# Kernel optimization log

Hardware: AMD Instinct MI355X
Metric: run time of the kernel (lower is better)

The kernel has to match this reference:

```python
import jax, jax.numpy as jnp
import numpy as np

SQRT_D = 32  # ceil(sqrt(d_out)) with d_out = 1024
D_OUT = 1024


def setup_inputs() -> dict:
    key = jax.random.key(0)
    k1, k2, k3 = jax.random.split(key, 3)
    x = jax.random.normal(k1, (8, 4096, 1024), dtype=jnp.float32)
    scale = 1.0 / np.sqrt(SQRT_D)
    L = jax.random.normal(k2, (SQRT_D, SQRT_D, SQRT_D), dtype=jnp.float32) * scale
    R = jax.random.normal(k3, (SQRT_D, SQRT_D, SQRT_D), dtype=jnp.float32) * scale
    return {"x": x, "L": L, "R": R}


def reference(x, L, R):
    # MonarchOutProjection with proj_type == 'Monarch' (d_in*n_heads == d_out,
    # hd == sqrt_d**2 so no padding). Monarch: permute -> blockdiag(L) ->
    # permute -> blockdiag(R) -> permute, then slice to d_out.
    b, n, hd = x.shape
    s = SQRT_D
    # rearrange '... (m n) -> ... (n m)': view (m, n) then transpose.
    h = x.reshape(b, n, s, s)          # (..., m, n_inner)
    h = jnp.swapaxes(h, -1, -2)        # (..., block, inner)
    # blockdiag_matmul with L: einsum 'bnm,...bm->...bn'
    h = jnp.einsum('bnm,...bm->...bn', L, h)
    # rearrange '... (m n) -> ... (n m)' on the flattened result == transpose
    h = jnp.swapaxes(h, -1, -2)
    # blockdiag_matmul with R
    h = jnp.einsum('bnm,...bm->...bn', R, h)
    # final rearrange '... (m n) -> ... (n m)'
    h = jnp.swapaxes(h, -1, -2)
    out = h.reshape(b, n, hd)
    return out[..., :D_OUT]
```

## Files before the change

kernel.cpp:

```cpp
#include <hip/hip_runtime.h>
#include <hip/hip_bf16.h>


typedef __attribute__((ext_vector_type(8))) short short8;
typedef __attribute__((ext_vector_type(4))) float floatx4;

__device__ __forceinline__ unsigned int f2bf(float f) {
    unsigned int u = __float_as_uint(f);
    return (u + 0x7fffu + ((u >> 16) & 1u)) >> 16;
}
__device__ __forceinline__ unsigned int pack2bf(float a, float b) {
    __hip_bfloat162 h = __float22bfloat162_rn(float2{a, b});
    return *(unsigned int*)&h;
}
__device__ __forceinline__ float bf2f(unsigned int u16) {
    return __uint_as_float(u16 << 16);
}

__global__ void prep_weights(const float* __restrict__ L, const float* __restrict__ R,
                             unsigned short* __restrict__ Lb, unsigned short* __restrict__ Rb) {
    const int t = blockIdx.x * 256 + threadIdx.x;
    const float* src        = (t < 4096) ? L : R;
    unsigned short* dst     = (t < 4096) ? Lb : Rb;
    const int i    = t & 4095;
    const int lane = i & 63;
    const int pq   = i >> 6;
    const int p    = pq >> 1;
    const int qt   = pq & 1;
    const int q    = qt * 16 + (lane & 15);
    const int m0   = (lane >> 4) * 8;
    const float* s = src + (p * 32 + q) * 32 + m0;
    uint4 o;
    o.x = pack2bf(s[0], s[1]);
    o.y = pack2bf(s[2], s[3]);
    o.z = pack2bf(s[4], s[5]);
    o.w = pack2bf(s[6], s[7]);
    *(uint4*)(dst + (size_t)i * 8) = o;
}

__global__ __launch_bounds__(256, 4)
void monarch_kernel(const float* __restrict__ x,
                    const unsigned short* __restrict__ Lb,
                    const unsigned short* __restrict__ Rb,
                    float* __restrict__ out) {
    __shared__ __align__(16) unsigned short buf[16][1024];

    const int tid  = threadIdx.x;
    const int w    = tid >> 6;
    const int lane = tid & 63;
    const int tl   = lane & 15;
    const int quad = lane >> 4;
    const long tok0 = (long)blockIdx.x * 16;

    {
        const int c = tid * 4;
        #pragma unroll
        for (int t = 0; t < 16; ++t) {
            const float4 v = *(const float4*)(x + (tok0 + t) * 1024 + c);
            *(unsigned int*)&buf[t][(c    ) ^ (2 * t)] = pack2bf(v.x, v.y);
            *(unsigned int*)&buf[t][(c + 2) ^ (2 * t)] = pack2bf(v.z, v.w);
        }
    }
    __syncthreads();

    {
        const int xsw = 2 * tl;
        #pragma unroll
        for (int pp = 0; pp < 8; ++pp) {
            const int p  = w * 8 + pp;
            const int pX = p ^ xsw;
            short8 b1;
            #pragma unroll
            for (int j = 0; j < 8; ++j)
                b1[j] = (short)buf[tl][quad * 256 + j * 32 + pX];
            #pragma unroll
            for (int qt = 0; qt < 2; ++qt) {
                const short8 a1 = *(const short8*)(Lb + (size_t)((p * 2 + qt) * 64 + lane) * 8);
                floatx4 acc = {0.f, 0.f, 0.f, 0.f};
                acc = __builtin_amdgcn_mfma_f32_16x16x32_bf16(a1, b1, acc, 0, 0, 0);
                #pragma unroll
                for (int r = 0; r < 4; ++r) {
                    const int qo = qt * 16 + quad * 4 + r;
                    buf[tl][qo * 32 + pX] = (unsigned short)f2bf(acc[r]);
                }
            }
        }
    }
    __syncthreads();

    floatx4 acc2[8][2];
    {
        const int xsw = 2 * tl;
        #pragma unroll
        for (int qq = 0; qq < 8; ++qq) {
            const int q = w * 8 + qq;
            short8 b2;
            #pragma unroll
            for (int j = 0; j < 8; ++j)
                b2[j] = (short)buf[tl][q * 32 + ((quad * 8 + j) ^ xsw)];
            #pragma unroll
            for (int rt = 0; rt < 2; ++rt) {
                const short8 a2 = *(const short8*)(Rb + (size_t)((q * 2 + rt) * 64 + lane) * 8);
                floatx4 z = {0.f, 0.f, 0.f, 0.f};
                acc2[qq][rt] = __builtin_amdgcn_mfma_f32_16x16x32_bf16(a2, b2, z, 0, 0, 0);
            }
        }
    }
    __syncthreads();

    {
        const int xsw = 2 * tl;
        #pragma unroll
        for (int qq = 0; qq < 8; ++qq) {
            const int q  = w * 8 + qq;
            const int qX = q ^ xsw;
            #pragma unroll
            for (int rt = 0; rt < 2; ++rt) {
                #pragma unroll
                for (int r4 = 0; r4 < 4; ++r4) {
                    const int ro = rt * 16 + quad * 4 + r4;
                    buf[tl][ro * 32 + qX] = (unsigned short)f2bf(acc2[qq][rt][r4]);
                }
            }
        }
    }
    __syncthreads();

    {
        const int c = tid * 4;
        #pragma unroll
        for (int t = 0; t < 16; ++t) {
            const unsigned int u0 = *(const unsigned int*)&buf[t][(c    ) ^ (2 * t)];
            const unsigned int u1 = *(const unsigned int*)&buf[t][(c + 2) ^ (2 * t)];
            float4 o;
            o.x = bf2f(u0 & 0xffffu); o.y = bf2f(u0 >> 16);
            o.z = bf2f(u1 & 0xffffu); o.w = bf2f(u1 >> 16);
            *(float4*)(out + (tok0 + t) * 1024 + c) = o;
        }
    }
}

extern "C" void kernel_launch(void* const* d_in, const int* in_sizes, int n_in,
                              void* d_out, int out_size, void* d_ws, size_t ws_size,
                              hipStream_t stream) {
    const float* x = (const float*)d_in[0];
    const float* L = (const float*)d_in[1];
    const float* R = (const float*)d_in[2];
    float* out = (float*)d_out;

    unsigned short* Lb = (unsigned short*)d_ws;
    unsigned short* Rb = Lb + 32768;

    prep_weights<<<32, 256, 0, stream>>>(L, R, Lb, Rb);

    const int n_tokens = 8 * 4096;
    const int grid = n_tokens / 16;
    monarch_kernel<<<grid, 256, 0, stream>>>(x, Lb, Rb, out);
}
```

Before: 241.6 us.

## Persist blocks over four token tiles with register prefetch and dual LDS buffers

```diff
diff --git a/kernel.cpp b/kernel.cpp
--- a/kernel.cpp
+++ b/kernel.cpp
@@ -5,16 +5,15 @@
 typedef __attribute__((ext_vector_type(8))) short short8;
 typedef __attribute__((ext_vector_type(4))) float floatx4;
 
-__device__ __forceinline__ unsigned int f2bf(float f) {
-    unsigned int u = __float_as_uint(f);
-    return (u + 0x7fffu + ((u >> 16) & 1u)) >> 16;
-}
 __device__ __forceinline__ unsigned int pack2bf(float a, float b) {
     __hip_bfloat162 h = __float22bfloat162_rn(float2{a, b});
     return *(unsigned int*)&h;
 }
-__device__ __forceinline__ float bf2f(unsigned int u16) {
-    return __uint_as_float(u16 << 16);
+
+__device__ __forceinline__ void block_sync() {
+    asm volatile("s_waitcnt lgkmcnt(0)" ::: "memory");
+    __builtin_amdgcn_s_barrier();
+    asm volatile("" ::: "memory");
 }
 
 __global__ void prep_weights(const float* __restrict__ L, const float* __restrict__ R,
@@ -38,105 +37,129 @@
     *(uint4*)(dst + (size_t)i * 8) = o;
 }
 
-__global__ __launch_bounds__(256, 4)
+#define TILES 4
+
+__global__ __launch_bounds__(256, 2)
 void monarch_kernel(const float* __restrict__ x,
                     const unsigned short* __restrict__ Lb,
                     const unsigned short* __restrict__ Rb,
                     float* __restrict__ out) {
-    __shared__ __align__(16) unsigned short buf[16][1024];
+    __shared__ __align__(16) unsigned short bufX[16][1024];
+    __shared__ __align__(16) unsigned short bufY[16][1024];
 
     const int tid  = threadIdx.x;
     const int w    = tid >> 6;
     const int lane = tid & 63;
     const int tl   = lane & 15;
     const int quad = lane >> 4;
-    const long tok0 = (long)blockIdx.x * 16;
+    const int c    = tid * 4;
 
+    short8 ra[8][2];
+    #pragma unroll
+    for (int qq = 0; qq < 8; ++qq) {
+        const int q = w * 8 + qq;
+        ra[qq][0] = *(const short8*)(Rb + (size_t)((q * 2 + 0) * 64 + lane) * 8);
+        ra[qq][1] = *(const short8*)(Rb + (size_t)((q * 2 + 1) * 64 + lane) * 8);
+    }
+
+    const long tile0 = (long)blockIdx.x * TILES;
+
+    float4 xr[16];
     {
-        const int c = tid * 4;
+        const long tok0 = tile0 * 16;
+        #pragma unroll
+        for (int t = 0; t < 16; ++t)
+            xr[t] = *(const float4*)(x + (tok0 + t) * 1024 + c);
+    }
+
+    for (int it = 0; it < TILES; ++it) {
+        const long tok0 = (tile0 + it) * 16;
+
+        short8 la[8][2];
+        #pragma unroll
+        for (int pp = 0; pp < 8; ++pp) {
+            const int p = w * 8 + pp;
+            la[pp][0] = *(const short8*)(Lb + (size_t)((p * 2 + 0) * 64 + lane) * 8);
+            la[pp][1] = *(const short8*)(Lb + (size_t)((p * 2 + 1) * 64 + lane) * 8);
+        }
+
         #pragma unroll
         for (int t = 0; t < 16; ++t) {
-            const float4 v = *(const float4*)(x + (tok0 + t) * 1024 + c);
-            *(unsigned int*)&buf[t][(c    ) ^ (2 * t)] = pack2bf(v.x, v.y);
-            *(unsigned int*)&buf[t][(c + 2) ^ (2 * t)] = pack2bf(v.z, v.w);
+            const unsigned long long v =
+                ((unsigned long long)pack2bf(xr[t].z, xr[t].w) << 32) | pack2bf(xr[t].x, xr[t].y);
+            *(unsigned long long*)&bufX[t][c ^ (t << 2)] = v;
         }
-    }
-    __syncthreads();
+        block_sync();
 
-    {
-        const int xsw = 2 * tl;
+        short8 b1[8];
         #pragma unroll
         for (int pp = 0; pp < 8; ++pp) {
-            const int p  = w * 8 + pp;
-            const int pX = p ^ xsw;
-            short8 b1;
+            const int p = w * 8 + pp;
             #pragma unroll
             for (int j = 0; j < 8; ++j)
-                b1[j] = (short)buf[tl][quad * 256 + j * 32 + pX];
+                b1[pp][j] = (short)bufX[tl][(quad * 256 + j * 32 + p) ^ (tl << 2)];
+        }
+        #pragma unroll
+        for (int pp = 0; pp < 8; ++pp) {
+            const int p = w * 8 + pp;
             #pragma unroll
             for (int qt = 0; qt < 2; ++qt) {
-                const short8 a1 = *(const short8*)(Lb + (size_t)((p * 2 + qt) * 64 + lane) * 8);
                 floatx4 acc = {0.f, 0.f, 0.f, 0.f};
-                acc = __builtin_amdgcn_mfma_f32_16x16x32_bf16(a1, b1, acc, 0, 0, 0);
-                #pragma unroll
-                for (int r = 0; r < 4; ++r) {
-                    const int qo = qt * 16 + quad * 4 + r;
-                    buf[tl][qo * 32 + pX] = (unsigned short)f2bf(acc[r]);
-                }
+                acc = __builtin_amdgcn_mfma_f32_16x16x32_bf16(la[pp][qt], b1[pp], acc, 0, 0, 0);
+                const unsigned long long v =
+                    ((unsigned long long)pack2bf(acc[2], acc[3]) << 32) | pack2bf(acc[0], acc[1]);
+                const int el = p * 32 + qt * 16 + quad * 4;
+                *(unsigned long long*)&bufY[tl][el ^ (tl << 2)] = v;
             }
         }
-    }
-    __syncthreads();
+        block_sync();
 
-    floatx4 acc2[8][2];
-    {
-        const int xsw = 2 * tl;
+        short8 b2[8];
         #pragma unroll
         for (int qq = 0; qq < 8; ++qq) {
             const int q = w * 8 + qq;
-            short8 b2;
             #pragma unroll
             for (int j = 0; j < 8; ++j)
-                b2[j] = (short)buf[tl][q * 32 + ((quad * 8 + j) ^ xsw)];
+                b2[qq][j] = (short)bufY[tl][((quad * 8 + j) * 32 + q) ^ (tl << 2)];
+        }
+        if (it + 1 < TILES) {
+            const long ntok0 = (tile0 + it + 1) * 16;
+            #pragma unroll
+            for (int t = 0; t < 16; ++t)
+                xr[t] = *(const float4*)(x + (ntok0 + t) * 1024 + c);
+        }
+        #pragma unroll
+        for (int qq = 0; qq < 8; ++qq) {
+            const int q = w * 8 + qq;
             #pragma unroll
             for (int rt = 0; rt < 2; ++rt) {
-                const short8 a2 = *(const short8*)(Rb + (size_t)((q * 2 + rt) * 64 + lane) * 8);
                 floatx4 z = {0.f, 0.f, 0.f, 0.f};
-                acc2[qq][rt] = __builtin_amdgcn_mfma_f32_16x16x32_bf16(a2, b2, z, 0, 0, 0);
+                const floatx4 acc =
+                    __builtin_amdgcn_mfma_f32_16x16x32_bf16(ra[qq][rt], b2[qq], z, 0, 0, 0);
+                const unsigned int lo = pack2bf(acc[0], acc[1]);
+                const unsigned int hi = pack2bf(acc[2], acc[3]);
+                const int r0 = rt * 16 + quad * 4;
+                bufX[tl][((r0    ) * 32 + q) ^ (tl << 2)] = (unsigned short)lo;
+                bufX[tl][((r0 + 1) * 32 + q) ^ (tl << 2)] = (unsigned short)(lo >> 16);
+                bufX[tl][((r0 + 2) * 32 + q) ^ (tl << 2)] = (unsigned short)hi;
+                bufX[tl][((r0 + 3) * 32 + q) ^ (tl << 2)] = (unsigned short)(hi >> 16);
             }
         }
-    }
-    __syncthreads();
+        block_sync();
 
-    {
-        const int xsw = 2 * tl;
-        #pragma unroll
-        for (int qq = 0; qq < 8; ++qq) {
-            const int q  = w * 8 + qq;
-            const int qX = q ^ xsw;
-            #pragma unroll
-            for (int rt = 0; rt < 2; ++rt) {
-                #pragma unroll
-                for (int r4 = 0; r4 < 4; ++r4) {
-                    const int ro = rt * 16 + quad * 4 + r4;
-                    buf[tl][ro * 32 + qX] = (unsigned short)f2bf(acc2[qq][rt][r4]);
-                }
-            }
-        }
-    }
-    __syncthreads();
-
-    {
-        const int c = tid * 4;
         #pragma unroll
         for (int t = 0; t < 16; ++t) {
-            const unsigned int u0 = *(const unsigned int*)&buf[t][(c    ) ^ (2 * t)];
-            const unsigned int u1 = *(const unsigned int*)&buf[t][(c + 2) ^ (2 * t)];
+            const unsigned long long v = *(const unsigned long long*)&bufX[t][c ^ (t << 2)];
+            const unsigned int lo = (unsigned int)v;
+            const unsigned int hi = (unsigned int)(v >> 32);
             float4 o;
-            o.x = bf2f(u0 & 0xffffu); o.y = bf2f(u0 >> 16);
-            o.z = bf2f(u1 & 0xffffu); o.w = bf2f(u1 >> 16);
+            o.x = __uint_as_float(lo << 16);
+            o.y = __uint_as_float(lo & 0xffff0000u);
+            o.z = __uint_as_float(hi << 16);
+            o.w = __uint_as_float(hi & 0xffff0000u);
             *(float4*)(out + (tok0 + t) * 1024 + c) = o;
         }
+        block_sync();
     }
 }
 
@@ -153,7 +176,5 @@
 
     prep_weights<<<32, 256, 0, stream>>>(L, R, Lb, Rb);
 
-    const int n_tokens = 8 * 4096;
-    const int grid = n_tokens / 16;
-    monarch_kernel<<<grid, 256, 0, stream>>>(x, Lb, Rb, out);
+    monarch_kernel<<<512, 256, 0, stream>>>(x, Lb, Rb, out);
 }
```

Measured after the change: 316.4 us. 1.31x slower.
